# Performance work log

Measured on AMD Instinct MI355X. Metric: run time of the kernel, lower is better.

Reference implementation:

```python
import jax, jax.numpy as jnp
import numpy as np

N = 100000      # nodes
E = 1200000     # edges
H = 64          # hidden_channels
L = 8           # num_layers
G = 100         # graphs in batch
ALPHA = 0.1
THETA = 0.5
EPS = 1e-5      # BatchNorm1d eps


def setup_inputs() -> dict:
    key = jax.random.key(0)
    ks = jax.random.split(key, 12)
    s = 0.05
    pos = jax.random.normal(ks[0], (N, 3), dtype=jnp.float32)
    edge_index = jax.random.randint(ks[1], (2, E), 0, N, dtype=jnp.int32)
    batch = jnp.sort(jax.random.randint(ks[2], (N,), 0, G, dtype=jnp.int32))
    return {
        "pos": pos,
        "edge_index": edge_index,
        "batch": batch,
        "lin0_w": jax.random.normal(ks[3], (3, H), dtype=jnp.float32) * s,
        "lin0_b": jnp.zeros((H,), jnp.float32),
        "conv_w": jax.random.normal(ks[4], (L, H, H), dtype=jnp.float32) * s,
        "lin1_w": jax.random.normal(ks[5], (H, H), dtype=jnp.float32) * s,
        "lin1_b": jnp.zeros((H,), jnp.float32),
        "mlp1_w": jax.random.normal(ks[6], (H, H), dtype=jnp.float32) * s,
        "mlp1_b": jnp.zeros((H,), jnp.float32),
        "bn1_g": jnp.ones((H,), jnp.float32),
        "bn1_b": jnp.zeros((H,), jnp.float32),
        "mlp2_w": jax.random.normal(ks[7], (H, H), dtype=jnp.float32) * s,
        "mlp2_b": jnp.zeros((H,), jnp.float32),
        "bn2_g": jnp.ones((H,), jnp.float32),
        "bn2_b": jnp.zeros((H,), jnp.float32),
        "out_w": jax.random.normal(ks[8], (H, 10), dtype=jnp.float32) * s,
        "out_b": jnp.zeros((10,), jnp.float32),
    }


def _bn(z, g, b):
    # BatchNorm1d, training-mode batch statistics
    mu = z.mean(axis=0)
    var = z.var(axis=0)
    return g * (z - mu) * jax.lax.rsqrt(var + EPS) + b


def reference(pos, edge_index, batch, lin0_w, lin0_b, conv_w, lin1_w, lin1_b,
              mlp1_w, mlp1_b, bn1_g, bn1_b, mlp2_w, mlp2_b, bn2_g, bn2_b,
              out_w, out_b):
    src, dst = edge_index[0], edge_index[1]
    x = jax.nn.relu(pos @ lin0_w + lin0_b)   # [N, H]
    x0 = x
    for l in range(L):
        beta = float(np.log(THETA / (l + 1) + 1.0))
        # GCN2Conv (normalize=False, shared_weights=True):
        # sum-aggregate neighbors, initial residual, identity mapping
        agg = jax.ops.segment_sum(x[src], dst, num_segments=N)   # [N, H]
        h = (1.0 - ALPHA) * agg + ALPHA * x0
        x = jax.nn.relu((1.0 - beta) * h + beta * (h @ conv_w[l]))
    x = x @ lin1_w + lin1_b
    pooled = jax.ops.segment_max(x, batch, num_segments=G)       # [G, H]
    pooled = jnp.where(jnp.isfinite(pooled), pooled, 0.0)        # guard empty segments
    h1 = jax.nn.relu(_bn(pooled @ mlp1_w + mlp1_b, bn1_g, bn1_b))
    h2 = jax.nn.relu(_bn(h1 @ mlp2_w + mlp2_b, bn2_g, bn2_b))
    logits = h2 @ out_w + out_b                                  # [G, 10]
    return jax.nn.log_softmax(logits, axis=-1)
```

## Files before the change

kernel.cpp:

```cpp
#include <hip/hip_runtime.h>
#include <math.h>

#define NNODES 100000
#define NEDGES 1200000
#define HD 64
#define NLAYERS 8
#define NGRAPH 100
#define PPART 32
#define C8 16777216.0f

typedef _Float16 f16;
typedef __attribute__((ext_vector_type(8))) _Float16 f16x8;
typedef __attribute__((ext_vector_type(4))) float f32x4;

__global__ void lin0_k(const float* __restrict__ pos, const float* __restrict__ w,
                       const float* __restrict__ b, float* __restrict__ x0f,
                       f16* __restrict__ x0h, int total) {
    int i = blockIdx.x * blockDim.x + threadIdx.x;
    if (i >= total) return;
    int n = i >> 6, h = i & 63;
    float p0 = pos[n * 3 + 0], p1 = pos[n * 3 + 1], p2 = pos[n * 3 + 2];
    float v = fmaf(p0, w[h], fmaf(p1, w[64 + h], fmaf(p2, w[128 + h], b[h])));
    v = fmaxf(v, 0.0f);
    x0f[i] = v;
    x0h[i] = (f16)v;
}

__global__ void hist_k(const int* __restrict__ dst, int* __restrict__ deg,
                       int* __restrict__ rank, int E) {
    int e = blockIdx.x * blockDim.x + threadIdx.x;
    if (e < E) rank[e] = atomicAdd(&deg[dst[e]], 1);
}

__global__ void scan_part_k(const int* __restrict__ deg, int* __restrict__ bsum, int n) {
    __shared__ int s[256];
    int t = threadIdx.x;
    int i = blockIdx.x * 256 + t;
    s[t] = (i < n) ? deg[i] : 0;
    __syncthreads();
    for (int off = 128; off > 0; off >>= 1) {
        if (t < off) s[t] += s[t + off];
        __syncthreads();
    }
    if (t == 0) bsum[blockIdx.x] = s[0];
}

__global__ void scan_mid_k(const int* __restrict__ bsum, int* __restrict__ boff,
                           int nblk, int* __restrict__ roff, int n) {
    __shared__ int s[512];
    int t = threadIdx.x;
    int v = (t < nblk) ? bsum[t] : 0;
    s[t] = v;
    __syncthreads();
    for (int off = 1; off < 512; off <<= 1) {
        int u = (t >= off) ? s[t - off] : 0;
        __syncthreads();
        s[t] += u;
        __syncthreads();
    }
    if (t < nblk) boff[t] = s[t] - v;
    if (t == nblk - 1) roff[n] = s[t];
}

__global__ void scan_final_k(const int* __restrict__ deg, const int* __restrict__ boff,
                             int* __restrict__ roff, int n) {
    __shared__ int s[256];
    int t = threadIdx.x;
    int i = blockIdx.x * 256 + t;
    int v = (i < n) ? deg[i] : 0;
    s[t] = v;
    __syncthreads();
    for (int off = 1; off < 256; off <<= 1) {
        int u = (t >= off) ? s[t - off] : 0;
        __syncthreads();
        s[t] += u;
        __syncthreads();
    }
    if (i < n) roff[i] = boff[blockIdx.x] + s[t] - v;
}

__global__ void fill_k(const int* __restrict__ src, const int* __restrict__ dst,
                       const int* __restrict__ roff, const int* __restrict__ rank,
                       int* __restrict__ csr, int E) {
    int e = blockIdx.x * blockDim.x + threadIdx.x;
    if (e < E) csr[roff[dst[e]] + rank[e]] = src[e];
}

__global__ void prep_k(const float* __restrict__ cw, f16* __restrict__ Bpack) {
    int t = blockIdx.x * blockDim.x + threadIdx.x;
    if (t >= NLAYERS * 4 * 2 * 64) return;
    int layer = t >> 9, rem = t & 511;
    int ct = rem >> 7, kk = (rem >> 6) & 1, lane = rem & 63;
    int g = lane >> 4, r = lane & 15;
    float beta = logf(0.5f / (float)(layer + 1) + 1.0f);
    const float* W = cw + (size_t)layer * 4096;
    f16* outp = Bpack + (size_t)t * 8;
    for (int j = 0; j < 8; ++j) {
        int row = 32 * kk + 8 * g + j;
        int col = 16 * ct + r;
        float m = beta * W[row * 64 + col];
        if (row == col) m += 1.0f - beta;
        outp[j] = (f16)(0.125f * m);
    }
}

__global__ __launch_bounds__(256, 8) void layer_k(
    const f16* __restrict__ xin, f16* __restrict__ xout,
    const float* __restrict__ x0, const f16* __restrict__ Bp,
    const int* __restrict__ roff, const int* __restrict__ csr,
    float x0scale, int nblocks) {
    __shared__ __align__(16) f16 Htile[16][72];
    const int tid   = threadIdx.x;
    const int lane  = tid & 63;
    const int wslot = tid >> 6;
    const f16x8 b0 = *(const f16x8*)(Bp + (size_t)((wslot * 2 + 0) * 64 + lane) * 8);
    const f16x8 b1 = *(const f16x8*)(Bp + (size_t)((wslot * 2 + 1) * 64 + lane) * 8);
    for (int tile = blockIdx.x; tile < NNODES / 16; tile += nblocks) {
        const int nbase = tile << 4;
#pragma unroll 1
        for (int i = 0; i < 4; ++i) {
            const int n = nbase + (wslot << 2) + i;
            const int beg = roff[n], end = roff[n + 1];
            float x0v = x0[(n << 6) + lane];
            float s0 = 0.0f, s1 = 0.0f, s2 = 0.0f, s3 = 0.0f;
            int e = beg;
            for (; e + 8 <= end; e += 8) {
                int e0 = csr[e + 0], e1 = csr[e + 1], e2 = csr[e + 2], e3 = csr[e + 3];
                int e4 = csr[e + 4], e5 = csr[e + 5], e6 = csr[e + 6], e7 = csr[e + 7];
                f16 a0 = xin[(e0 << 6) + lane];
                f16 a1 = xin[(e1 << 6) + lane];
                f16 a2 = xin[(e2 << 6) + lane];
                f16 a3 = xin[(e3 << 6) + lane];
                f16 a4 = xin[(e4 << 6) + lane];
                f16 a5 = xin[(e5 << 6) + lane];
                f16 a6 = xin[(e6 << 6) + lane];
                f16 a7 = xin[(e7 << 6) + lane];
                s0 += (float)a0; s1 += (float)a1; s2 += (float)a2; s3 += (float)a3;
                s0 += (float)a4; s1 += (float)a5; s2 += (float)a6; s3 += (float)a7;
            }
            for (; e + 4 <= end; e += 4) {
                int e0 = csr[e + 0], e1 = csr[e + 1], e2 = csr[e + 2], e3 = csr[e + 3];
                s0 += (float)xin[(e0 << 6) + lane];
                s1 += (float)xin[(e1 << 6) + lane];
                s2 += (float)xin[(e2 << 6) + lane];
                s3 += (float)xin[(e3 << 6) + lane];
            }
            for (; e < end; ++e) s0 += (float)xin[(csr[e] << 6) + lane];
            float h = fmaf(0.9f, (s0 + s1) + (s2 + s3), x0scale * x0v);
            Htile[(wslot << 2) + i][lane] = (f16)h;
        }
        __syncthreads();
        const int ar = lane & 15, ag = lane >> 4;
        f16x8 a0 = *(const f16x8*)&Htile[ar][(ag << 3) + 0];
        f16x8 a1 = *(const f16x8*)&Htile[ar][(ag << 3) + 32];
        f32x4 acc = {0.0f, 0.0f, 0.0f, 0.0f};
        acc = __builtin_amdgcn_mfma_f32_16x16x32_f16(a0, b0, acc, 0, 0, 0);
        acc = __builtin_amdgcn_mfma_f32_16x16x32_f16(a1, b1, acc, 0, 0, 0);
        const int col = (wslot << 4) + ar;
        const int rbase = nbase + (ag << 2);
#pragma unroll
        for (int j = 0; j < 4; ++j) {
            xout[((rbase + j) << 6) + col] = (f16)fmaxf(acc[j], 0.0f);
        }
        __syncthreads();
    }
}

__device__ __forceinline__ int lbound(const int* __restrict__ a, int n, int v) {
    int lo = 0, hi = n;
    while (lo < hi) { int mid = (lo + hi) >> 1; if (a[mid] < v) lo = mid + 1; else hi = mid; }
    return lo;
}

__global__ __launch_bounds__(256, 8) void poolpart_k(
    const f16* __restrict__ xin, const float* __restrict__ W,
    const float* __restrict__ bvec, const int* __restrict__ batch,
    float* __restrict__ pmax) {
    __shared__ __align__(16) float MT[64 * 64];
    __shared__ __align__(16) float hrow[4][64];
    __shared__ float wm[4][64];
    const int tid   = threadIdx.x;
    const int lane  = tid & 63;
    const int wslot = tid >> 6;
    for (int idx = tid; idx < 4096; idx += 256) {
        int k = idx >> 6, j = idx & 63;
        MT[j * 64 + (((k >> 2) ^ (j & 15)) << 2) + (k & 3)] = W[idx];
    }
    __syncthreads();
    const int g = blockIdx.x / PPART, part = blockIdx.x % PPART;
    const int lo = lbound(batch, NNODES, g);
    const int hi = lbound(batch, NNODES, g + 1);
    const int cnt = hi - lo;
    const int qlo = lo + (cnt * part) / PPART;
    const int qhi = lo + (cnt * (part + 1)) / PPART;
    const float bias = bvec[lane];
    float vmax = -INFINITY;
    for (int n = qlo + wslot; n < qhi; n += 4) {
        hrow[wslot][lane] = (float)xin[(n << 6) + lane];
        __builtin_amdgcn_wave_barrier();
        float a0 = 0.0f, a1 = 0.0f, a2 = 0.0f, a3 = 0.0f;
#pragma unroll
        for (int gg = 0; gg < 16; ++gg) {
            float4 hv = *(const float4*)&hrow[wslot][gg * 4];
            float4 mv = *(const float4*)&MT[(lane << 6) + ((gg ^ (lane & 15)) << 2)];
            a0 = fmaf(hv.x, mv.x, a0);
            a1 = fmaf(hv.y, mv.y, a1);
            a2 = fmaf(hv.z, mv.z, a2);
            a3 = fmaf(hv.w, mv.w, a3);
        }
        __builtin_amdgcn_wave_barrier();
        float acc = (a0 + a1) + (a2 + a3);
        vmax = fmaxf(vmax, fmaf(C8, acc, bias));
    }
    wm[wslot][lane] = vmax;
    __syncthreads();
    if (tid < 64) {
        float m = fmaxf(fmaxf(wm[0][tid], wm[1][tid]), fmaxf(wm[2][tid], wm[3][tid]));
        pmax[blockIdx.x * 64 + tid] = m;
    }
}

__global__ void poolcomb_k(const float* __restrict__ pmax, float* __restrict__ pooled) {
    int i = blockIdx.x * blockDim.x + threadIdx.x;
    if (i >= NGRAPH * 64) return;
    int g = i >> 6, lane = i & 63;
    float m = -INFINITY;
    for (int p = 0; p < PPART; ++p)
        m = fmaxf(m, pmax[(PPART * g + p) * 64 + lane]);
    pooled[i] = m;
}

__global__ __launch_bounds__(256) void head_k(
    const float* __restrict__ pooled,
    const float* __restrict__ m1w, const float* __restrict__ m1b,
    const float* __restrict__ g1, const float* __restrict__ be1,
    const float* __restrict__ m2w, const float* __restrict__ m2b,
    const float* __restrict__ g2, const float* __restrict__ be2,
    const float* __restrict__ ow, const float* __restrict__ ob,
    float* __restrict__ out) {
    __shared__ float A[NGRAPH * 64];
    __shared__ float B[NGRAPH * 64];
    __shared__ float mu[64], rs[64];
    __shared__ float LG[NGRAPH * 10];
    int t = threadIdx.x;
    for (int i = t; i < NGRAPH * 64; i += 256) {
        float f = pooled[i];
        if (!isfinite(f)) f = 0.0f;
        A[i] = f;
    }
    __syncthreads();
    for (int i = t; i < NGRAPH * 64; i += 256) {
        int g = i >> 6, j = i & 63;
        float acc = m1b[j];
        for (int k = 0; k < 64; ++k) acc = fmaf(A[(g << 6) + k], m1w[k * 64 + j], acc);
        B[i] = acc;
    }
    __syncthreads();
    if (t < 64) {
        float sm = 0.0f, sq = 0.0f;
        for (int g = 0; g < NGRAPH; ++g) { float z = B[g * 64 + t]; sm += z; sq += z * z; }
        float m = sm * (1.0f / NGRAPH);
        float var = sq * (1.0f / NGRAPH) - m * m;
        mu[t] = m; rs[t] = rsqrtf(var + 1e-5f);
    }
    __syncthreads();
    for (int i = t; i < NGRAPH * 64; i += 256) {
        int j = i & 63;
        float z = fmaf((B[i] - mu[j]) * rs[j], g1[j], be1[j]);
        A[i] = fmaxf(z, 0.0f);
    }
    __syncthreads();
    for (int i = t; i < NGRAPH * 64; i += 256) {
        int g = i >> 6, j = i & 63;
        float acc = m2b[j];
        for (int k = 0; k < 64; ++k) acc = fmaf(A[(g << 6) + k], m2w[k * 64 + j], acc);
        B[i] = acc;
    }
    __syncthreads();
    if (t < 64) {
        float sm = 0.0f, sq = 0.0f;
        for (int g = 0; g < NGRAPH; ++g) { float z = B[g * 64 + t]; sm += z; sq += z * z; }
        float m = sm * (1.0f / NGRAPH);
        float var = sq * (1.0f / NGRAPH) - m * m;
        mu[t] = m; rs[t] = rsqrtf(var + 1e-5f);
    }
    __syncthreads();
    for (int i = t; i < NGRAPH * 64; i += 256) {
        int j = i & 63;
        float z = fmaf((B[i] - mu[j]) * rs[j], g2[j], be2[j]);
        A[i] = fmaxf(z, 0.0f);
    }
    __syncthreads();
    for (int i = t; i < NGRAPH * 10; i += 256) {
        int g = i / 10, j = i - g * 10;
        float acc = ob[j];
        for (int k = 0; k < 64; ++k) acc = fmaf(A[(g << 6) + k], ow[k * 10 + j], acc);
        LG[i] = acc;
    }
    __syncthreads();
    if (t < NGRAPH) {
        float m = -1e30f;
        for (int j = 0; j < 10; ++j) m = fmaxf(m, LG[t * 10 + j]);
        float s = 0.0f;
        for (int j = 0; j < 10; ++j) s += expf(LG[t * 10 + j] - m);
        float lse = m + logf(s);
        for (int j = 0; j < 10; ++j) out[t * 10 + j] = LG[t * 10 + j] - lse;
    }
}

extern "C" void kernel_launch(void* const* d_in, const int* in_sizes, int n_in,
                              void* d_out, int out_size, void* d_ws, size_t ws_size,
                              hipStream_t stream) {
    const float* pos   = (const float*)d_in[0];
    const int*   eidx  = (const int*)d_in[1];
    const int*   batch = (const int*)d_in[2];
    const float* l0w   = (const float*)d_in[3];
    const float* l0b   = (const float*)d_in[4];
    const float* cw    = (const float*)d_in[5];
    const float* l1w   = (const float*)d_in[6];
    const float* l1b   = (const float*)d_in[7];
    const float* m1w   = (const float*)d_in[8];
    const float* m1b   = (const float*)d_in[9];
    const float* g1    = (const float*)d_in[10];
    const float* b1    = (const float*)d_in[11];
    const float* m2w   = (const float*)d_in[12];
    const float* m2b   = (const float*)d_in[13];
    const float* g2    = (const float*)d_in[14];
    const float* b2    = (const float*)d_in[15];
    const float* ow    = (const float*)d_in[16];
    const float* ob    = (const float*)d_in[17];
    float* out = (float*)d_out;
    const int* src = eidx;
    const int* dst = eidx + NEDGES;

    size_t off = 0;
    auto alloc = [&](size_t bytes) -> void* {
        void* p = (char*)d_ws + off;
        off += (bytes + 255) & ~(size_t)255;
        return p;
    };
    float* x0f    = (float*)alloc((size_t)NNODES * 64 * 4);
    f16*   x0h    = (f16*)alloc((size_t)NNODES * 64 * 2);
    f16*   xA     = (f16*)alloc((size_t)NNODES * 64 * 2);
    f16*   xB     = (f16*)alloc((size_t)NNODES * 64 * 2);
    int*   deg    = (int*)alloc((size_t)NNODES * 4);
    int*   roff   = (int*)alloc((size_t)(NNODES + 1) * 4);
    const int NBLK = (NNODES + 255) / 256;
    int*   bsum   = (int*)alloc((size_t)NBLK * 4);
    int*   boff   = (int*)alloc((size_t)NBLK * 4);
    int*   csr    = (int*)alloc((size_t)NEDGES * 4);
    float* pooled = (float*)alloc((size_t)NGRAPH * 64 * 4);
    float* pmax   = (float*)alloc((size_t)NGRAPH * PPART * 64 * 4);
    f16*   Bpack  = (f16*)alloc((size_t)NLAYERS * 4 * 2 * 64 * 8 * 2);
    int*   rank   = (int*)xB;

    hipMemsetAsync(deg, 0, (size_t)NNODES * 4, stream);
    {
        int total = NNODES * 64;
        lin0_k<<<(total + 255) / 256, 256, 0, stream>>>(pos, l0w, l0b, x0f, x0h, total);
    }
    hist_k<<<(NEDGES + 255) / 256, 256, 0, stream>>>(dst, deg, rank, NEDGES);
    scan_part_k<<<NBLK, 256, 0, stream>>>(deg, bsum, NNODES);
    scan_mid_k<<<1, 512, 0, stream>>>(bsum, boff, NBLK, roff, NNODES);
    scan_final_k<<<NBLK, 256, 0, stream>>>(deg, boff, roff, NNODES);
    fill_k<<<(NEDGES + 255) / 256, 256, 0, stream>>>(src, dst, roff, rank, csr, NEDGES);
    prep_k<<<(NLAYERS * 4 * 2 * 64 + 255) / 256, 256, 0, stream>>>(cw, Bpack);

    const int LBLOCKS = 2048;
    const f16* cur = x0h;
    for (int l = 0; l < NLAYERS; ++l) {
        float x0scale = (float)(0.1 * ldexp(1.0, -3 * l));
        f16* nxt = (l & 1) ? xB : xA;
        layer_k<<<LBLOCKS, 256, 0, stream>>>(cur, nxt, x0f,
                                             Bpack + (size_t)l * 4 * 2 * 64 * 8,
                                             roff, csr, x0scale, LBLOCKS);
        cur = nxt;
    }
    poolpart_k<<<NGRAPH * PPART, 256, 0, stream>>>(cur, l1w, l1b, batch, pmax);
    poolcomb_k<<<(NGRAPH * 64 + 255) / 256, 256, 0, stream>>>(pmax, pooled);
    head_k<<<1, 256, 0, stream>>>(pooled, m1w, m1b, g1, b1, m2w, m2b, g2, b2, ow, ob, out);
}
```

Before: 565.7 us.

## Move lin1 to MFMA kernel, defer bias past max, store x0 as fp16

The fp32 LDS matvec in the pooling kernel is replaced by a separate MFMA-based lin1 kernel that writes fp16 outputs. The pooling kernel then reduces to a plain segment max, and the C8 scale and bias are applied after the max in the combine step. The fp32 copy of x0 is dropped and each layer reads the fp16 x0, which cuts per-layer read traffic and the lin0 writes. The cost is an extra kernel pass over the node features, plus fp16 rounding of x0 and of the lin1 outputs.

```diff
diff --git a/kernel.cpp b/kernel.cpp
--- a/kernel.cpp
+++ b/kernel.cpp
@@ -14,16 +14,13 @@
 typedef __attribute__((ext_vector_type(4))) float f32x4;
 
 __global__ void lin0_k(const float* __restrict__ pos, const float* __restrict__ w,
-                       const float* __restrict__ b, float* __restrict__ x0f,
-                       f16* __restrict__ x0h, int total) {
+                       const float* __restrict__ b, f16* __restrict__ x0h, int total) {
     int i = blockIdx.x * blockDim.x + threadIdx.x;
     if (i >= total) return;
     int n = i >> 6, h = i & 63;
     float p0 = pos[n * 3 + 0], p1 = pos[n * 3 + 1], p2 = pos[n * 3 + 2];
     float v = fmaf(p0, w[h], fmaf(p1, w[64 + h], fmaf(p2, w[128 + h], b[h])));
-    v = fmaxf(v, 0.0f);
-    x0f[i] = v;
-    x0h[i] = (f16)v;
+    x0h[i] = (f16)fmaxf(v, 0.0f);
 }
 
 __global__ void hist_k(const int* __restrict__ dst, int* __restrict__ deg,
@@ -86,27 +83,36 @@
     if (e < E) csr[roff[dst[e]] + rank[e]] = src[e];
 }
 
-__global__ void prep_k(const float* __restrict__ cw, f16* __restrict__ Bpack) {
+__global__ void prep_k(const float* __restrict__ cw, const float* __restrict__ l1w,
+                       f16* __restrict__ Bpack) {
     int t = blockIdx.x * blockDim.x + threadIdx.x;
-    if (t >= NLAYERS * 4 * 2 * 64) return;
-    int layer = t >> 9, rem = t & 511;
+    if (t >= 9 * 4 * 2 * 64) return;
+    int mat = t >> 9, rem = t & 511;
     int ct = rem >> 7, kk = (rem >> 6) & 1, lane = rem & 63;
     int g = lane >> 4, r = lane & 15;
-    float beta = logf(0.5f / (float)(layer + 1) + 1.0f);
-    const float* W = cw + (size_t)layer * 4096;
     f16* outp = Bpack + (size_t)t * 8;
-    for (int j = 0; j < 8; ++j) {
-        int row = 32 * kk + 8 * g + j;
-        int col = 16 * ct + r;
-        float m = beta * W[row * 64 + col];
-        if (row == col) m += 1.0f - beta;
-        outp[j] = (f16)(0.125f * m);
+    if (mat < 8) {
+        float beta = logf(0.5f / (float)(mat + 1) + 1.0f);
+        const float* W = cw + (size_t)mat * 4096;
+        for (int j = 0; j < 8; ++j) {
+            int row = 32 * kk + 8 * g + j;
+            int col = 16 * ct + r;
+            float m = beta * W[row * 64 + col];
+            if (row == col) m += 1.0f - beta;
+            outp[j] = (f16)(0.125f * m);
+        }
+    } else {
+        for (int j = 0; j < 8; ++j) {
+            int row = 32 * kk + 8 * g + j;
+            int col = 16 * ct + r;
+            outp[j] = (f16)l1w[row * 64 + col];
+        }
     }
 }
 
 __global__ __launch_bounds__(256, 8) void layer_k(
     const f16* __restrict__ xin, f16* __restrict__ xout,
-    const float* __restrict__ x0, const f16* __restrict__ Bp,
+    const f16* __restrict__ x0, const f16* __restrict__ Bp,
     const int* __restrict__ roff, const int* __restrict__ csr,
     float x0scale, int nblocks) {
     __shared__ __align__(16) f16 Htile[16][72];
@@ -121,7 +127,7 @@
         for (int i = 0; i < 4; ++i) {
             const int n = nbase + (wslot << 2) + i;
             const int beg = roff[n], end = roff[n + 1];
-            float x0v = x0[(n << 6) + lane];
+            float x0v = (float)x0[(n << 6) + lane];
             float s0 = 0.0f, s1 = 0.0f, s2 = 0.0f, s3 = 0.0f;
             int e = beg;
             for (; e + 8 <= end; e += 8) {
@@ -166,52 +172,52 @@
     }
 }
 
+__global__ __launch_bounds__(256, 8) void lin1_k(
+    const f16* __restrict__ xin, f16* __restrict__ yout,
+    const f16* __restrict__ Bp, int nblocks) {
+    const int lane  = threadIdx.x & 63;
+    const int wslot = threadIdx.x >> 6;
+    const f16x8 b0 = *(const f16x8*)(Bp + (size_t)((wslot * 2 + 0) * 64 + lane) * 8);
+    const f16x8 b1 = *(const f16x8*)(Bp + (size_t)((wslot * 2 + 1) * 64 + lane) * 8);
+    const int ar = lane & 15, ag = lane >> 4;
+    for (int tile = blockIdx.x; tile < NNODES / 16; tile += nblocks) {
+        const int nbase = tile << 4;
+        f16x8 a0 = *(const f16x8*)(xin + ((size_t)(nbase + ar) << 6) + (ag << 3));
+        f16x8 a1 = *(const f16x8*)(xin + ((size_t)(nbase + ar) << 6) + (ag << 3) + 32);
+        f32x4 acc = {0.0f, 0.0f, 0.0f, 0.0f};
+        acc = __builtin_amdgcn_mfma_f32_16x16x32_f16(a0, b0, acc, 0, 0, 0);
+        acc = __builtin_amdgcn_mfma_f32_16x16x32_f16(a1, b1, acc, 0, 0, 0);
+        const int col = (wslot << 4) + ar;
+        const int rbase = nbase + (ag << 2);
+#pragma unroll
+        for (int j = 0; j < 4; ++j) {
+            yout[((rbase + j) << 6) + col] = (f16)acc[j];
+        }
+    }
+}
+
 __device__ __forceinline__ int lbound(const int* __restrict__ a, int n, int v) {
     int lo = 0, hi = n;
     while (lo < hi) { int mid = (lo + hi) >> 1; if (a[mid] < v) lo = mid + 1; else hi = mid; }
     return lo;
 }
 
-__global__ __launch_bounds__(256, 8) void poolpart_k(
-    const f16* __restrict__ xin, const float* __restrict__ W,
-    const float* __restrict__ bvec, const int* __restrict__ batch,
+__global__ __launch_bounds__(256, 8) void segmax_k(
+    const f16* __restrict__ y, const int* __restrict__ batch,
     float* __restrict__ pmax) {
-    __shared__ __align__(16) float MT[64 * 64];
-    __shared__ __align__(16) float hrow[4][64];
     __shared__ float wm[4][64];
     const int tid   = threadIdx.x;
     const int lane  = tid & 63;
     const int wslot = tid >> 6;
-    for (int idx = tid; idx < 4096; idx += 256) {
-        int k = idx >> 6, j = idx & 63;
-        MT[j * 64 + (((k >> 2) ^ (j & 15)) << 2) + (k & 3)] = W[idx];
-    }
-    __syncthreads();
     const int g = blockIdx.x / PPART, part = blockIdx.x % PPART;
     const int lo = lbound(batch, NNODES, g);
     const int hi = lbound(batch, NNODES, g + 1);
     const int cnt = hi - lo;
     const int qlo = lo + (cnt * part) / PPART;
     const int qhi = lo + (cnt * (part + 1)) / PPART;
-    const float bias = bvec[lane];
     float vmax = -INFINITY;
-    for (int n = qlo + wslot; n < qhi; n += 4) {
-        hrow[wslot][lane] = (float)xin[(n << 6) + lane];
-        __builtin_amdgcn_wave_barrier();
-        float a0 = 0.0f, a1 = 0.0f, a2 = 0.0f, a3 = 0.0f;
-#pragma unroll
-        for (int gg = 0; gg < 16; ++gg) {
-            float4 hv = *(const float4*)&hrow[wslot][gg * 4];
-            float4 mv = *(const float4*)&MT[(lane << 6) + ((gg ^ (lane & 15)) << 2)];
-            a0 = fmaf(hv.x, mv.x, a0);
-            a1 = fmaf(hv.y, mv.y, a1);
-            a2 = fmaf(hv.z, mv.z, a2);
-            a3 = fmaf(hv.w, mv.w, a3);
-        }
-        __builtin_amdgcn_wave_barrier();
-        float acc = (a0 + a1) + (a2 + a3);
-        vmax = fmaxf(vmax, fmaf(C8, acc, bias));
-    }
+    for (int n = qlo + wslot; n < qhi; n += 4)
+        vmax = fmaxf(vmax, (float)y[(n << 6) + lane]);
     wm[wslot][lane] = vmax;
     __syncthreads();
     if (tid < 64) {
@@ -220,14 +226,16 @@
     }
 }
 
-__global__ void poolcomb_k(const float* __restrict__ pmax, float* __restrict__ pooled) {
+__global__ void poolcomb_k(const float* __restrict__ pmax,
+                           const float* __restrict__ bvec,
+                           float* __restrict__ pooled) {
     int i = blockIdx.x * blockDim.x + threadIdx.x;
     if (i >= NGRAPH * 64) return;
     int g = i >> 6, lane = i & 63;
     float m = -INFINITY;
     for (int p = 0; p < PPART; ++p)
         m = fmaxf(m, pmax[(PPART * g + p) * 64 + lane]);
-    pooled[i] = m;
+    pooled[i] = fmaf(C8, m, bvec[lane]);
 }
 
 __global__ __launch_bounds__(256) void head_k(
@@ -339,7 +347,6 @@
         off += (bytes + 255) & ~(size_t)255;
         return p;
     };
-    float* x0f    = (float*)alloc((size_t)NNODES * 64 * 4);
     f16*   x0h    = (f16*)alloc((size_t)NNODES * 64 * 2);
     f16*   xA     = (f16*)alloc((size_t)NNODES * 64 * 2);
     f16*   xB     = (f16*)alloc((size_t)NNODES * 64 * 2);
@@ -351,32 +358,35 @@
     int*   csr    = (int*)alloc((size_t)NEDGES * 4);
     float* pooled = (float*)alloc((size_t)NGRAPH * 64 * 4);
     float* pmax   = (float*)alloc((size_t)NGRAPH * PPART * 64 * 4);
-    f16*   Bpack  = (f16*)alloc((size_t)NLAYERS * 4 * 2 * 64 * 8 * 2);
+    f16*   Bpack  = (f16*)alloc((size_t)9 * 4 * 2 * 64 * 8 * 2);
     int*   rank   = (int*)xB;
 
     hipMemsetAsync(deg, 0, (size_t)NNODES * 4, stream);
     {
         int total = NNODES * 64;
-        lin0_k<<<(total + 255) / 256, 256, 0, stream>>>(pos, l0w, l0b, x0f, x0h, total);
+        lin0_k<<<(total + 255) / 256, 256, 0, stream>>>(pos, l0w, l0b, x0h, total);
     }
     hist_k<<<(NEDGES + 255) / 256, 256, 0, stream>>>(dst, deg, rank, NEDGES);
     scan_part_k<<<NBLK, 256, 0, stream>>>(deg, bsum, NNODES);
     scan_mid_k<<<1, 512, 0, stream>>>(bsum, boff, NBLK, roff, NNODES);
     scan_final_k<<<NBLK, 256, 0, stream>>>(deg, boff, roff, NNODES);
     fill_k<<<(NEDGES + 255) / 256, 256, 0, stream>>>(src, dst, roff, rank, csr, NEDGES);
-    prep_k<<<(NLAYERS * 4 * 2 * 64 + 255) / 256, 256, 0, stream>>>(cw, Bpack);
+    prep_k<<<(9 * 4 * 2 * 64 + 255) / 256, 256, 0, stream>>>(cw, l1w, Bpack);
 
     const int LBLOCKS = 2048;
     const f16* cur = x0h;
     for (int l = 0; l < NLAYERS; ++l) {
         float x0scale = (float)(0.1 * ldexp(1.0, -3 * l));
         f16* nxt = (l & 1) ? xB : xA;
-        layer_k<<<LBLOCKS, 256, 0, stream>>>(cur, nxt, x0f,
+        layer_k<<<LBLOCKS, 256, 0, stream>>>(cur, nxt, x0h,
                                              Bpack + (size_t)l * 4 * 2 * 64 * 8,
                                              roff, csr, x0scale, LBLOCKS);
         cur = nxt;
     }
-    poolpart_k<<<NGRAPH * PPART, 256, 0, stream>>>(cur, l1w, l1b, batch, pmax);
-    poolcomb_k<<<(NGRAPH * 64 + 255) / 256, 256, 0, stream>>>(pmax, pooled);
+    f16* l1out = (cur == xA) ? xB : xA;
+    lin1_k<<<LBLOCKS, 256, 0, stream>>>(cur, l1out,
+                                        Bpack + (size_t)8 * 4 * 2 * 64 * 8, LBLOCKS);
+    segmax_k<<<NGRAPH * PPART, 256, 0, stream>>>(l1out, batch, pmax);
+    poolcomb_k<<<(NGRAPH * 64 + 255) / 256, 256, 0, stream>>>(pmax, l1b, pooled);
     head_k<<<1, 256, 0, stream>>>(pooled, m1w, m1b, g1, b1, m2w, m2b, g2, b2, ow, ob, out);
 }
```

New measurement: 545.7 us. 3.5% less time.
